# Performance work log

Measured on AMD Instinct MI355X. Metric: run time of the kernel, lower is better.

Reference implementation:

```python
import jax, jax.numpy as jnp
import numpy as np

N_SRC = 50000
N_DST = 50000
N_EDGES = 800000
D = 128
H = 128


def setup_inputs() -> dict:
    key = jax.random.key(0)
    ks = jax.random.split(key, 10)
    return {
        "feat_src": jax.random.normal(ks[0], (N_SRC, D), dtype=jnp.float32),
        "feat_dst": jax.random.normal(ks[1], (N_DST, D), dtype=jnp.float32),
        "W1": jax.random.normal(ks[2], (H, D), dtype=jnp.float32) * 0.05,
        "b1": jnp.zeros((H,), dtype=jnp.float32),
        "W2": jax.random.normal(ks[3], (H, 3 * D), dtype=jnp.float32) * 0.05,
        "b2": jnp.zeros((H,), dtype=jnp.float32),
        "W3": jax.random.normal(ks[4], (H, 2 * H), dtype=jnp.float32) * 0.05,
        "b3": jnp.zeros((H,), dtype=jnp.float32),
        "src_idx": jax.random.randint(ks[5], (N_EDGES,), 0, N_SRC, dtype=jnp.int32),
        "dst_idx": jax.random.randint(ks[6], (N_EDGES,), 0, N_DST, dtype=jnp.int32),
    }


def reference(feat_src, feat_dst, W1, b1, W2, b2, W3, b3, src_idx, dst_idx):
    n_dst = feat_dst.shape[0]
    # copy_u: gather source features along edges  [E, D]
    m = feat_src[src_idx]
    # fn.max -> 'max'; NOTE: source code's 'mean' is ALSO fn.max (faithful to bug)
    mx = jax.ops.segment_max(m, dst_idx, num_segments=n_dst)
    mx = jnp.where(jnp.isfinite(mx), mx, jnp.zeros_like(mx))  # zero-degree dst -> 0 (DGL convention)
    sm = jax.ops.segment_sum(m, dst_idx, num_segments=n_dst)
    agg = jnp.concatenate([mx, mx, sm], axis=1)  # [N_dst, 3D]
    z2 = agg @ W2.T + b2            # fc2
    z1 = feat_dst @ W1.T + b1       # fc1
    h = jax.nn.relu(jnp.concatenate([z2, z1], axis=1))  # [N_dst, 2H]
    out = jax.nn.relu(h @ W3.T + b3)  # fc3 = Linear + ReLU
    return out
```

## Files before the change

kernel.cpp:

```cpp
#include <hip/hip_runtime.h>
#include <math.h>

#define NDST 50000
#define NSRC 50000
#define NEDGE 800000
#define DF 128

#define NBUK 1563
#define NCH 128
#define EPC (NEDGE / NCH)
#define HN (NBUK * NCH)
#define CAP 1536

typedef __attribute__((ext_vector_type(4))) float f32x4;
typedef __attribute__((ext_vector_type(8))) short bf16x8;

__device__ __forceinline__ ushort f2bf(float f) {
    union { float f; unsigned int u; } c; c.f = f;
    unsigned int u = c.u;
    unsigned int r = (u + 0x7fffu + ((u >> 16) & 1u)) >> 16;
    return (ushort)r;
}
__device__ __forceinline__ float bflo(unsigned int u) {
    union { unsigned int u; float f; } c; c.u = u << 16; return c.f;
}
__device__ __forceinline__ float bfhi(unsigned int u) {
    union { unsigned int u; float f; } c; c.u = u & 0xffff0000u; return c.f;
}

__global__ void zero_hist(uint4* __restrict__ hist4) {
    int i = blockIdx.x * 256 + threadIdx.x;
    if (i < HN / 4) hist4[i] = make_uint4(0, 0, 0, 0);
}

__global__ void hist_k(const int* __restrict__ dst_idx, int* __restrict__ hist) {
    int c = blockIdx.x, tid = threadIdx.x;
    int base = c * EPC;
    for (int e = base + tid; e < base + EPC; e += 256)
        atomicAdd(&hist[(dst_idx[e] >> 5) * NCH + c], 1);
}

__global__ void scan_bsums(const int* __restrict__ a, int* __restrict__ bsum, int n) {
    __shared__ int ws[4];
    int i = blockIdx.x * 256 + threadIdx.x;
    int v = (i < n) ? a[i] : 0;
    #pragma unroll
    for (int off = 32; off > 0; off >>= 1) v += __shfl_down(v, off, 64);
    if ((threadIdx.x & 63) == 0) ws[threadIdx.x >> 6] = v;
    __syncthreads();
    if (threadIdx.x == 0) bsum[blockIdx.x] = ws[0] + ws[1] + ws[2] + ws[3];
}

__global__ __launch_bounds__(256)
void scan_mid(const int* __restrict__ bsum, int* __restrict__ bpre, int nb) {
    __shared__ int part[256];
    int t = threadIdx.x;
    int ch = (nb + 255) / 256;
    int lo = t * ch, hi = min(nb, lo + ch);
    int s = 0;
    for (int i = lo; i < hi; ++i) s += bsum[i];
    part[t] = s;
    __syncthreads();
    for (int off = 1; off < 256; off <<= 1) {
        int v = (t >= off) ? part[t - off] : 0;
        __syncthreads();
        part[t] += v;
        __syncthreads();
    }
    int run = (t == 0) ? 0 : part[t - 1];
    for (int i = lo; i < hi; ++i) { bpre[i] = run; run += bsum[i]; }
}

__global__ __launch_bounds__(256)
void scan_final(const int* __restrict__ a, const int* __restrict__ bpre,
                int* __restrict__ out, int n) {
    __shared__ int s[256];
    int b = blockIdx.x, t = threadIdx.x;
    int i = b * 256 + t;
    int v = (i < n) ? a[i] : 0;
    s[t] = v;
    __syncthreads();
    for (int off = 1; off < 256; off <<= 1) {
        int u = (t >= off) ? s[t - off] : 0;
        __syncthreads();
        s[t] += u;
        __syncthreads();
    }
    if (i < n) out[i] = bpre[b] + s[t] - v;
}

__global__ __launch_bounds__(256)
void partition_k(const int* __restrict__ src_idx, const int* __restrict__ dst_idx,
                 const int* __restrict__ scanned, unsigned int* __restrict__ pairs) {
    __shared__ int offs_l[NBUK];
    int c = blockIdx.x, tid = threadIdx.x;
    for (int i = tid; i < NBUK; i += 256) offs_l[i] = scanned[i * NCH + c];
    __syncthreads();
    int base = c * EPC;
    for (int e = base + tid; e < base + EPC; e += 256) {
        int d = dst_idx[e];
        int pos = atomicAdd(&offs_l[d >> 5], 1);
        pairs[pos] = (unsigned int)src_idx[e] | ((unsigned int)(d & 31) << 16);
    }
}

__global__ void conv_fs(const float* __restrict__ fs, unsigned int* __restrict__ fs_b) {
    int i = blockIdx.x * 256 + threadIdx.x;
    if (i >= NSRC * DF / 4) return;
    float4 v = *(const float4*)(fs + (size_t)i * 4);
    unsigned int lo = (unsigned int)f2bf(v.x) | ((unsigned int)f2bf(v.y) << 16);
    unsigned int hi = (unsigned int)f2bf(v.z) | ((unsigned int)f2bf(v.w) << 16);
    *(uint2*)(fs_b + (size_t)i * 2) = make_uint2(lo, hi);
}

__global__ void prep_weights(const float* __restrict__ W2, const float* __restrict__ W1,
                             const float* __restrict__ W3,
                             ushort* __restrict__ Wz_b, ushort* __restrict__ W1_b,
                             ushort* __restrict__ W3_b) {
    int i = blockIdx.x * 256 + threadIdx.x;
    if (i < 128 * 256) {
        int c = i >> 8, k = i & 255;
        float v = (k < 128) ? (W2[c * 384 + k] + W2[c * 384 + 128 + k])
                            : W2[c * 384 + 128 + k];
        Wz_b[i] = f2bf(v);
    } else if (i < 128 * 256 + 128 * 128) {
        int j = i - 128 * 256;
        W1_b[j] = f2bf(W1[j]);
    } else if (i < 128 * 256 + 128 * 128 + 128 * 256) {
        int j = i - 128 * 256 - 128 * 128;
        W3_b[j] = f2bf(W3[j]);
    }
}

__global__ __launch_bounds__(256)
void bucket_sort_agg(const unsigned int* __restrict__ fs_b,
                     const unsigned int* __restrict__ pairs,
                     const int* __restrict__ scanned,
                     unsigned int* __restrict__ mx_b, unsigned int* __restrict__ sm_b) {
    __shared__ int s_src[CAP];
    __shared__ int s_cnt[32], s_off[32], s_cur[32];
    int B = blockIdx.x, tid = threadIdx.x;
    int w = tid >> 6, lane = tid & 63;
    int s0 = scanned[B * NCH];
    int s1 = (B + 1 < NBUK) ? scanned[(B + 1) * NCH] : NEDGE;

    float mx0[8], mx1[8], sm0[8], sm1[8];
    #pragma unroll
    for (int j = 0; j < 8; ++j) {
        mx0[j] = -INFINITY; mx1[j] = -INFINITY; sm0[j] = 0.f; sm1[j] = 0.f;
    }

    for (int cs = s0; cs < s1; cs += CAP) {
        int n = min(CAP, s1 - cs);
        if (tid < 32) s_cnt[tid] = 0;
        __syncthreads();
        for (int i = tid; i < n; i += 256)
            atomicAdd(&s_cnt[(pairs[cs + i] >> 16) & 31u], 1);
        __syncthreads();
        if (tid < 32) {
            int v = s_cnt[tid];
            int incl = v;
            #pragma unroll
            for (int d = 1; d < 32; d <<= 1) {
                int o = __shfl_up(incl, d, 64);
                if (tid >= d) incl += o;
            }
            s_off[tid] = incl - v;
            s_cur[tid] = incl - v;
        }
        __syncthreads();
        for (int i = tid; i < n; i += 256) {
            unsigned int p = pairs[cs + i];
            int pos = atomicAdd(&s_cur[(p >> 16) & 31u], 1);
            s_src[pos] = (int)(p & 0xFFFFu);
        }
        __syncthreads();
        #pragma unroll
        for (int j = 0; j < 8; ++j) {
            int dl = w * 8 + j;
            int e = s_off[dl], eend = e + s_cnt[dl];
            for (; e + 3 < eend; e += 4) {
                int i0 = s_src[e], i1 = s_src[e + 1], i2 = s_src[e + 2], i3 = s_src[e + 3];
                unsigned int u0 = fs_b[(size_t)i0 * 64 + lane];
                unsigned int u1 = fs_b[(size_t)i1 * 64 + lane];
                unsigned int u2 = fs_b[(size_t)i2 * 64 + lane];
                unsigned int u3 = fs_b[(size_t)i3 * 64 + lane];
                float a0 = bflo(u0), c0 = bfhi(u0);
                float a1 = bflo(u1), c1 = bfhi(u1);
                float a2 = bflo(u2), c2 = bfhi(u2);
                float a3 = bflo(u3), c3 = bfhi(u3);
                mx0[j] = fmaxf(fmaxf(fmaxf(mx0[j], a0), a1), fmaxf(a2, a3));
                mx1[j] = fmaxf(fmaxf(fmaxf(mx1[j], c0), c1), fmaxf(c2, c3));
                sm0[j] += (a0 + a1) + (a2 + a3);
                sm1[j] += (c0 + c1) + (c2 + c3);
            }
            for (; e < eend; ++e) {
                unsigned int u = fs_b[(size_t)s_src[e] * 64 + lane];
                float a = bflo(u), c = bfhi(u);
                mx0[j] = fmaxf(mx0[j], a);
                mx1[j] = fmaxf(mx1[j], c);
                sm0[j] += a;
                sm1[j] += c;
            }
        }
        __syncthreads();
    }

    int base_d = B * 32;
    #pragma unroll
    for (int j = 0; j < 8; ++j) {
        int d = base_d + w * 8 + j;
        if (d >= NDST) continue;
        float m0 = mx0[j], m1 = mx1[j];
        if (m0 == -INFINITY) m0 = 0.f;
        if (m1 == -INFINITY) m1 = 0.f;
        union { float f; unsigned int u; } c0, c1;
        c0.f = m0; c1.f = m1;
        size_t o = (size_t)d * 64 + lane;
        mx_b[o] = (c0.u >> 16) | (c1.u & 0xFFFF0000u);
        sm_b[o] = (unsigned int)f2bf(sm0[j]) | ((unsigned int)f2bf(sm1[j]) << 16);
    }
}

#define GBM 128
#define GBK 32
#define LDW 40

template <int ABF, int OBF>
__global__ __launch_bounds__(256)
void gemm_mfma(const void* __restrict__ a0v, int a0s,
               const void* __restrict__ a1v, int a1s,
               const ushort* __restrict__ Wb,
               const float* __restrict__ bias,
               void* __restrict__ Cv, int ldc, int coloff,
               int M, int K) {
    __shared__ ushort As[GBM * LDW];
    __shared__ ushort Ws[128 * LDW];
    int tid = threadIdx.x;
    int bm = blockIdx.x * GBM;
    int wid = tid >> 6, lane = tid & 63;
    int wm = (wid & 1) * 64, wn = (wid >> 1) * 64;
    int lrow = lane & 15, lk8 = (lane >> 4) * 8;

    f32x4 acc[4][4];
    #pragma unroll
    for (int i = 0; i < 4; ++i)
        #pragma unroll
        for (int j = 0; j < 4; ++j)
            acc[i][j] = (f32x4){0.f, 0.f, 0.f, 0.f};

    int sr = tid >> 1;
    int skh = (tid & 1) * 16;

    for (int k0 = 0; k0 < K; k0 += GBK) {
        int part = k0 >> 7;
        int kl = (k0 & 127) + skh;
        int m = bm + sr;
        uint4 w0, w1;
        if (ABF) {
            const ushort* ap = part ? (const ushort*)a1v : (const ushort*)a0v;
            int as = part ? a1s : a0s;
            if (m < M) {
                const ushort* p = ap + (size_t)m * as + kl;
                w0 = *(const uint4*)p;
                w1 = *(const uint4*)(p + 8);
            } else {
                w0 = make_uint4(0, 0, 0, 0); w1 = w0;
            }
        } else {
            const float* ap = part ? (const float*)a1v : (const float*)a0v;
            int as = part ? a1s : a0s;
            unsigned int pk[8];
            if (m < M) {
                const float* p = ap + (size_t)m * as + kl;
                #pragma unroll
                for (int j = 0; j < 8; ++j) {
                    float x = p[2 * j], y = p[2 * j + 1];
                    pk[j] = (unsigned int)f2bf(x) | ((unsigned int)f2bf(y) << 16);
                }
            } else {
                #pragma unroll
                for (int j = 0; j < 8; ++j) pk[j] = 0;
            }
            w0 = make_uint4(pk[0], pk[1], pk[2], pk[3]);
            w1 = make_uint4(pk[4], pk[5], pk[6], pk[7]);
        }
        *(uint4*)&As[sr * LDW + skh] = w0;
        *(uint4*)&As[sr * LDW + skh + 8] = w1;

        const ushort* wp = Wb + (size_t)sr * K + k0 + skh;
        uint4 v0 = *(const uint4*)wp;
        uint4 v1 = *(const uint4*)(wp + 8);
        *(uint4*)&Ws[sr * LDW + skh] = v0;
        *(uint4*)&Ws[sr * LDW + skh + 8] = v1;
        __syncthreads();

        bf16x8 af[4], bfr[4];
        #pragma unroll
        for (int mi = 0; mi < 4; ++mi)
            af[mi] = *(const bf16x8*)&As[(wm + mi * 16 + lrow) * LDW + lk8];
        #pragma unroll
        for (int ni = 0; ni < 4; ++ni)
            bfr[ni] = *(const bf16x8*)&Ws[(wn + ni * 16 + lrow) * LDW + lk8];
        #pragma unroll
        for (int mi = 0; mi < 4; ++mi)
            #pragma unroll
            for (int ni = 0; ni < 4; ++ni)
                acc[mi][ni] = __builtin_amdgcn_mfma_f32_16x16x32_bf16(
                    af[mi], bfr[ni], acc[mi][ni], 0, 0, 0);
        __syncthreads();
    }

    int rbase = (lane >> 4) * 4;
    #pragma unroll
    for (int ni = 0; ni < 4; ++ni) {
        int n = wn + ni * 16 + lrow;
        float bv = bias[n];
        #pragma unroll
        for (int mi = 0; mi < 4; ++mi) {
            #pragma unroll
            for (int r = 0; r < 4; ++r) {
                int m = bm + wm + mi * 16 + rbase + r;
                if (m < M) {
                    float v = fmaxf(acc[mi][ni][r] + bv, 0.f);
                    if (OBF) ((ushort*)Cv)[(size_t)m * ldc + coloff + n] = f2bf(v);
                    else     ((float*)Cv)[(size_t)m * ldc + coloff + n] = v;
                }
            }
        }
    }
}

extern "C" void kernel_launch(void* const* d_in, const int* in_sizes, int n_in,
                              void* d_out, int out_size, void* d_ws, size_t ws_size,
                              hipStream_t stream) {
    const float* feat_src = (const float*)d_in[0];
    const float* feat_dst = (const float*)d_in[1];
    const float* W1 = (const float*)d_in[2];
    const float* b1 = (const float*)d_in[3];
    const float* W2 = (const float*)d_in[4];
    const float* b2 = (const float*)d_in[5];
    const float* W3 = (const float*)d_in[6];
    const float* b3 = (const float*)d_in[7];
    const int* src_idx = (const int*)d_in[8];
    const int* dst_idx = (const int*)d_in[9];

    float* out = (float*)d_out;

    unsigned int* fs_b = (unsigned int*)d_ws;
    unsigned int* mx_b = fs_b + (size_t)NSRC * 64;
    unsigned int* sm_b = mx_b + (size_t)NDST * 64;
    ushort* h_b  = (ushort*)(sm_b + (size_t)NDST * 64);
    ushort* Wz_b = h_b + (size_t)NDST * 256;
    ushort* W1_b = Wz_b + 128 * 256;
    ushort* W3_b = W1_b + 128 * 128;
    int* hist    = (int*)(W3_b + 128 * 256);
    int* scanned = hist + HN;
    int* bsum    = scanned + HN;
    int* bpre    = bsum + 1024;
    unsigned int* pairs = (unsigned int*)(bpre + 1024);

    const int NBH = (HN + 255) / 256;

    zero_hist<<<(HN / 4 + 255) / 256, 256, 0, stream>>>((uint4*)hist);
    hist_k<<<NCH, 256, 0, stream>>>(dst_idx, hist);
    scan_bsums<<<NBH, 256, 0, stream>>>(hist, bsum, HN);
    scan_mid<<<1, 256, 0, stream>>>(bsum, bpre, NBH);
    scan_final<<<NBH, 256, 0, stream>>>(hist, bpre, scanned, HN);
    partition_k<<<NCH, 256, 0, stream>>>(src_idx, dst_idx, scanned, pairs);

    conv_fs<<<(NSRC * DF / 4 + 255) / 256, 256, 0, stream>>>(feat_src, fs_b);
    prep_weights<<<(128 * 256 * 2 + 128 * 128 + 255) / 256, 256, 0, stream>>>(
        W2, W1, W3, Wz_b, W1_b, W3_b);

    dim3 ggrid((NDST + GBM - 1) / GBM, 1);
    gemm_mfma<0, 1><<<ggrid, 256, 0, stream>>>(feat_dst, DF, nullptr, 0,
                                               W1_b, b1, h_b, 256, 128, NDST, 128);

    bucket_sort_agg<<<NBUK, 256, 0, stream>>>(fs_b, pairs, scanned, mx_b, sm_b);

    gemm_mfma<1, 1><<<ggrid, 256, 0, stream>>>(mx_b, DF, sm_b, DF,
                                               Wz_b, b2, h_b, 256, 0, NDST, 256);
    gemm_mfma<1, 0><<<ggrid, 256, 0, stream>>>(h_b, 256, h_b + 128, 256,
                                               W3_b, b3, out, DF, 0, NDST, 256);
}
```

Measured before the change: 169.8 us.

## Fuse three MLP GEMMs into one kernel and merge prep kernels

Replaces the three separate GEMM launches (fc1, fc2, fc3) with one fused kernel. Each 64-row tile computes the hidden activations for fc2 and fc1 into shared memory, then runs fc3 directly from there, so the bf16 hidden buffer no longer round-trips through global memory. Feature conversion, histogram zeroing and weight preparation are also merged into a single launch. The cost is a smaller M tile with more shared memory per block and serialized phases inside each block, which may lower occupancy and MFMA reuse.

```diff
diff --git a/kernel.cpp b/kernel.cpp
--- a/kernel.cpp
+++ b/kernel.cpp
@@ -28,9 +28,41 @@
     union { unsigned int u; float f; } c; c.u = u & 0xffff0000u; return c.f;
 }
 
-__global__ void zero_hist(uint4* __restrict__ hist4) {
-    int i = blockIdx.x * 256 + threadIdx.x;
-    if (i < HN / 4) hist4[i] = make_uint4(0, 0, 0, 0);
+#define NB_CONV 6250
+#define NB_ZERO 196
+#define NB_PREP 320
+
+__global__ void prep_all(const float* __restrict__ fs, unsigned int* __restrict__ fs_b,
+                         uint4* __restrict__ hist4,
+                         const float* __restrict__ W2, const float* __restrict__ W1,
+                         const float* __restrict__ W3,
+                         ushort* __restrict__ Wz_b, ushort* __restrict__ W1_b,
+                         ushort* __restrict__ W3_b) {
+    int b = blockIdx.x, tid = threadIdx.x;
+    if (b < NB_CONV) {
+        int i = b * 256 + tid;
+        float4 v = *(const float4*)(fs + (size_t)i * 4);
+        unsigned int lo = (unsigned int)f2bf(v.x) | ((unsigned int)f2bf(v.y) << 16);
+        unsigned int hi = (unsigned int)f2bf(v.z) | ((unsigned int)f2bf(v.w) << 16);
+        *(uint2*)(fs_b + (size_t)i * 2) = make_uint2(lo, hi);
+    } else if (b < NB_CONV + NB_ZERO) {
+        int i = (b - NB_CONV) * 256 + tid;
+        if (i < HN / 4) hist4[i] = make_uint4(0, 0, 0, 0);
+    } else {
+        int i = (b - NB_CONV - NB_ZERO) * 256 + tid;
+        if (i < 128 * 256) {
+            int c = i >> 8, k = i & 255;
+            float v = (k < 128) ? (W2[c * 384 + k] + W2[c * 384 + 128 + k])
+                                : W2[c * 384 + 128 + k];
+            Wz_b[i] = f2bf(v);
+        } else if (i < 128 * 256 + 128 * 128) {
+            int j = i - 128 * 256;
+            W1_b[j] = f2bf(W1[j]);
+        } else if (i < 128 * 256 + 128 * 128 + 128 * 256) {
+            int j = i - 128 * 256 - 128 * 128;
+            W3_b[j] = f2bf(W3[j]);
+        }
+    }
 }
 
 __global__ void hist_k(const int* __restrict__ dst_idx, int* __restrict__ hist) {
@@ -101,34 +133,6 @@
         int d = dst_idx[e];
         int pos = atomicAdd(&offs_l[d >> 5], 1);
         pairs[pos] = (unsigned int)src_idx[e] | ((unsigned int)(d & 31) << 16);
-    }
-}
-
-__global__ void conv_fs(const float* __restrict__ fs, unsigned int* __restrict__ fs_b) {
-    int i = blockIdx.x * 256 + threadIdx.x;
-    if (i >= NSRC * DF / 4) return;
-    float4 v = *(const float4*)(fs + (size_t)i * 4);
-    unsigned int lo = (unsigned int)f2bf(v.x) | ((unsigned int)f2bf(v.y) << 16);
-    unsigned int hi = (unsigned int)f2bf(v.z) | ((unsigned int)f2bf(v.w) << 16);
-    *(uint2*)(fs_b + (size_t)i * 2) = make_uint2(lo, hi);
-}
-
-__global__ void prep_weights(const float* __restrict__ W2, const float* __restrict__ W1,
-                             const float* __restrict__ W3,
-                             ushort* __restrict__ Wz_b, ushort* __restrict__ W1_b,
-                             ushort* __restrict__ W3_b) {
-    int i = blockIdx.x * 256 + threadIdx.x;
-    if (i < 128 * 256) {
-        int c = i >> 8, k = i & 255;
-        float v = (k < 128) ? (W2[c * 384 + k] + W2[c * 384 + 128 + k])
-                            : W2[c * 384 + 128 + k];
-        Wz_b[i] = f2bf(v);
-    } else if (i < 128 * 256 + 128 * 128) {
-        int j = i - 128 * 256;
-        W1_b[j] = f2bf(W1[j]);
-    } else if (i < 128 * 256 + 128 * 128 + 128 * 256) {
-        int j = i - 128 * 256 - 128 * 128;
-        W3_b[j] = f2bf(W3[j]);
     }
 }
 
@@ -222,112 +226,136 @@
     }
 }
 
-#define GBM 128
-#define GBK 32
+#define BM2 64
 #define LDW 40
-
-template <int ABF, int OBF>
+#define LDH 264
+
 __global__ __launch_bounds__(256)
-void gemm_mfma(const void* __restrict__ a0v, int a0s,
-               const void* __restrict__ a1v, int a1s,
-               const ushort* __restrict__ Wb,
-               const float* __restrict__ bias,
-               void* __restrict__ Cv, int ldc, int coloff,
-               int M, int K) {
-    __shared__ ushort As[GBM * LDW];
+void mlp_fused(const ushort* __restrict__ mxa, const ushort* __restrict__ sma,
+               const float* __restrict__ feat_dst,
+               const ushort* __restrict__ Wz_b, const ushort* __restrict__ W1_b,
+               const ushort* __restrict__ W3_b,
+               const float* __restrict__ b1, const float* __restrict__ b2,
+               const float* __restrict__ b3,
+               float* __restrict__ out) {
+    __shared__ ushort Hs[BM2 * LDH];
+    __shared__ ushort As[BM2 * LDW];
     __shared__ ushort Ws[128 * LDW];
     int tid = threadIdx.x;
-    int bm = blockIdx.x * GBM;
+    int bm = blockIdx.x * BM2;
     int wid = tid >> 6, lane = tid & 63;
-    int wm = (wid & 1) * 64, wn = (wid >> 1) * 64;
+    int wm = (wid & 1) * 32, wn = (wid >> 1) * 64;
     int lrow = lane & 15, lk8 = (lane >> 4) * 8;
-
-    f32x4 acc[4][4];
-    #pragma unroll
-    for (int i = 0; i < 4; ++i)
+    int rbase = (lane >> 4) * 4;
+
+    int sra = tid >> 2, ska = (tid & 3) * 8;
+    int srw = tid >> 1, skw = (tid & 1) * 16;
+
+    f32x4 acc[2][4];
+
+    #pragma unroll
+    for (int half = 0; half < 2; ++half) {
+        #pragma unroll
+        for (int i = 0; i < 2; ++i)
+            #pragma unroll
+            for (int j = 0; j < 4; ++j)
+                acc[i][j] = (f32x4){0.f, 0.f, 0.f, 0.f};
+        int K = half ? 128 : 256;
+        const ushort* Wb = half ? W1_b : Wz_b;
+        for (int k0 = 0; k0 < K; k0 += 32) {
+            int m = bm + sra;
+            uint4 av = make_uint4(0, 0, 0, 0);
+            if (m < NDST) {
+                if (half == 0) {
+                    const ushort* ap = (k0 < 128) ? mxa : sma;
+                    av = *(const uint4*)(ap + (size_t)m * 128 + (k0 & 127) + ska);
+                } else {
+                    const float* p = feat_dst + (size_t)m * 128 + k0 + ska;
+                    unsigned int pk[4];
+                    #pragma unroll
+                    for (int j = 0; j < 4; ++j) {
+                        float x = p[2 * j], y = p[2 * j + 1];
+                        pk[j] = (unsigned int)f2bf(x) | ((unsigned int)f2bf(y) << 16);
+                    }
+                    av = make_uint4(pk[0], pk[1], pk[2], pk[3]);
+                }
+            }
+            *(uint4*)&As[sra * LDW + ska] = av;
+
+            const ushort* wp = Wb + (size_t)srw * K + k0 + skw;
+            *(uint4*)&Ws[srw * LDW + skw] = *(const uint4*)wp;
+            *(uint4*)&Ws[srw * LDW + skw + 8] = *(const uint4*)(wp + 8);
+            __syncthreads();
+
+            bf16x8 af[2], bfr[4];
+            #pragma unroll
+            for (int mi = 0; mi < 2; ++mi)
+                af[mi] = *(const bf16x8*)&As[(wm + mi * 16 + lrow) * LDW + lk8];
+            #pragma unroll
+            for (int ni = 0; ni < 4; ++ni)
+                bfr[ni] = *(const bf16x8*)&Ws[(wn + ni * 16 + lrow) * LDW + lk8];
+            #pragma unroll
+            for (int mi = 0; mi < 2; ++mi)
+                #pragma unroll
+                for (int ni = 0; ni < 4; ++ni)
+                    acc[mi][ni] = __builtin_amdgcn_mfma_f32_16x16x32_bf16(
+                        af[mi], bfr[ni], acc[mi][ni], 0, 0, 0);
+            __syncthreads();
+        }
+        const float* bias = half ? b1 : b2;
+        #pragma unroll
+        for (int ni = 0; ni < 4; ++ni) {
+            int n = wn + ni * 16 + lrow;
+            float bv = bias[n];
+            #pragma unroll
+            for (int mi = 0; mi < 2; ++mi)
+                #pragma unroll
+                for (int r = 0; r < 4; ++r) {
+                    float v = fmaxf(acc[mi][ni][r] + bv, 0.f);
+                    Hs[(wm + mi * 16 + rbase + r) * LDH + half * 128 + n] = f2bf(v);
+                }
+        }
+    }
+    __syncthreads();
+
+    #pragma unroll
+    for (int i = 0; i < 2; ++i)
         #pragma unroll
         for (int j = 0; j < 4; ++j)
             acc[i][j] = (f32x4){0.f, 0.f, 0.f, 0.f};
-
-    int sr = tid >> 1;
-    int skh = (tid & 1) * 16;
-
-    for (int k0 = 0; k0 < K; k0 += GBK) {
-        int part = k0 >> 7;
-        int kl = (k0 & 127) + skh;
-        int m = bm + sr;
-        uint4 w0, w1;
-        if (ABF) {
-            const ushort* ap = part ? (const ushort*)a1v : (const ushort*)a0v;
-            int as = part ? a1s : a0s;
-            if (m < M) {
-                const ushort* p = ap + (size_t)m * as + kl;
-                w0 = *(const uint4*)p;
-                w1 = *(const uint4*)(p + 8);
-            } else {
-                w0 = make_uint4(0, 0, 0, 0); w1 = w0;
-            }
-        } else {
-            const float* ap = part ? (const float*)a1v : (const float*)a0v;
-            int as = part ? a1s : a0s;
-            unsigned int pk[8];
-            if (m < M) {
-                const float* p = ap + (size_t)m * as + kl;
-                #pragma unroll
-                for (int j = 0; j < 8; ++j) {
-                    float x = p[2 * j], y = p[2 * j + 1];
-                    pk[j] = (unsigned int)f2bf(x) | ((unsigned int)f2bf(y) << 16);
-                }
-            } else {
-                #pragma unroll
-                for (int j = 0; j < 8; ++j) pk[j] = 0;
-            }
-            w0 = make_uint4(pk[0], pk[1], pk[2], pk[3]);
-            w1 = make_uint4(pk[4], pk[5], pk[6], pk[7]);
-        }
-        *(uint4*)&As[sr * LDW + skh] = w0;
-        *(uint4*)&As[sr * LDW + skh + 8] = w1;
-
-        const ushort* wp = Wb + (size_t)sr * K + k0 + skh;
-        uint4 v0 = *(const uint4*)wp;
-        uint4 v1 = *(const uint4*)(wp + 8);
-        *(uint4*)&Ws[sr * LDW + skh] = v0;
-        *(uint4*)&Ws[sr * LDW + skh + 8] = v1;
-        __syncthreads();
-
-        bf16x8 af[4], bfr[4];
-        #pragma unroll
-        for (int mi = 0; mi < 4; ++mi)
-            af[mi] = *(const bf16x8*)&As[(wm + mi * 16 + lrow) * LDW + lk8];
+    for (int k0 = 0; k0 < 256; k0 += 32) {
+        const ushort* wp = W3_b + (size_t)srw * 256 + k0 + skw;
+        *(uint4*)&Ws[srw * LDW + skw] = *(const uint4*)wp;
+        *(uint4*)&Ws[srw * LDW + skw + 8] = *(const uint4*)(wp + 8);
+        __syncthreads();
+
+        bf16x8 af[2], bfr[4];
+        #pragma unroll
+        for (int mi = 0; mi < 2; ++mi)
+            af[mi] = *(const bf16x8*)&Hs[(wm + mi * 16 + lrow) * LDH + k0 + lk8];
         #pragma unroll
         for (int ni = 0; ni < 4; ++ni)
             bfr[ni] = *(const bf16x8*)&Ws[(wn + ni * 16 + lrow) * LDW + lk8];
         #pragma unroll
-        for (int mi = 0; mi < 4; ++mi)
+        for (int mi = 0; mi < 2; ++mi)
             #pragma unroll
             for (int ni = 0; ni < 4; ++ni)
                 acc[mi][ni] = __builtin_amdgcn_mfma_f32_16x16x32_bf16(
                     af[mi], bfr[ni], acc[mi][ni], 0, 0, 0);
         __syncthreads();
     }
-
-    int rbase = (lane >> 4) * 4;
     #pragma unroll
     for (int ni = 0; ni < 4; ++ni) {
         int n = wn + ni * 16 + lrow;
-        float bv = bias[n];
-        #pragma unroll
-        for (int mi = 0; mi < 4; ++mi) {
+        float bv = b3[n];
+        #pragma unroll
+        for (int mi = 0; mi < 2; ++mi)
             #pragma unroll
             for (int r = 0; r < 4; ++r) {
                 int m = bm + wm + mi * 16 + rbase + r;
-                if (m < M) {
-                    float v = fmaxf(acc[mi][ni][r] + bv, 0.f);
-                    if (OBF) ((ushort*)Cv)[(size_t)m * ldc + coloff + n] = f2bf(v);
-                    else     ((float*)Cv)[(size_t)m * ldc + coloff + n] = v;
-                }
+                if (m < NDST)
+                    out[(size_t)m * 128 + n] = fmaxf(acc[mi][ni][r] + bv, 0.f);
             }
-        }
     }
 }
 
@@ -350,8 +378,7 @@
     unsigned int* fs_b = (unsigned int*)d_ws;
     unsigned int* mx_b = fs_b + (size_t)NSRC * 64;
     unsigned int* sm_b = mx_b + (size_t)NDST * 64;
-    ushort* h_b  = (ushort*)(sm_b + (size_t)NDST * 64);
-    ushort* Wz_b = h_b + (size_t)NDST * 256;
+    ushort* Wz_b = (ushort*)(sm_b + (size_t)NDST * 64);
     ushort* W1_b = Wz_b + 128 * 256;
     ushort* W3_b = W1_b + 128 * 128;
     int* hist    = (int*)(W3_b + 128 * 256);
@@ -362,25 +389,18 @@
 
     const int NBH = (HN + 255) / 256;
 
-    zero_hist<<<(HN / 4 + 255) / 256, 256, 0, stream>>>((uint4*)hist);
+    prep_all<<<NB_CONV + NB_ZERO + NB_PREP, 256, 0, stream>>>(
+        feat_src, fs_b, (uint4*)hist, W2, W1, W3, Wz_b, W1_b, W3_b);
+
     hist_k<<<NCH, 256, 0, stream>>>(dst_idx, hist);
     scan_bsums<<<NBH, 256, 0, stream>>>(hist, bsum, HN);
     scan_mid<<<1, 256, 0, stream>>>(bsum, bpre, NBH);
     scan_final<<<NBH, 256, 0, stream>>>(hist, bpre, scanned, HN);
     partition_k<<<NCH, 256, 0, stream>>>(src_idx, dst_idx, scanned, pairs);
 
-    conv_fs<<<(NSRC * DF / 4 + 255) / 256, 256, 0, stream>>>(feat_src, fs_b);
-    prep_weights<<<(128 * 256 * 2 + 128 * 128 + 255) / 256, 256, 0, stream>>>(
-        W2, W1, W3, Wz_b, W1_b, W3_b);
-
-    dim3 ggrid((NDST + GBM - 1) / GBM, 1);
-    gemm_mfma<0, 1><<<ggrid, 256, 0, stream>>>(feat_dst, DF, nullptr, 0,
-                                               W1_b, b1, h_b, 256, 128, NDST, 128);
-
     bucket_sort_agg<<<NBUK, 256, 0, stream>>>(fs_b, pairs, scanned, mx_b, sm_b);
 
-    gemm_mfma<1, 1><<<ggrid, 256, 0, stream>>>(mx_b, DF, sm_b, DF,
-                                               Wz_b, b2, h_b, 256, 0, NDST, 256);
-    gemm_mfma<1, 0><<<ggrid, 256, 0, stream>>>(h_b, 256, h_b + 128, 256,
-                                               W3_b, b3, out, DF, 0, NDST, 256);
-}
+    mlp_fused<<<(NDST + BM2 - 1) / BM2, 256, 0, stream>>>(
+        (const ushort*)mx_b, (const ushort*)sm_b, feat_dst,
+        Wz_b, W1_b, W3_b, b1, b2, b3, out);
+}
```

Measured after the change: 146.6 us. 1.16x faster.
